# Performance work log

Hardware: AMD Instinct MI355X
Metric: run time of the kernel (lower is better)

## Reference

```python
import jax, jax.numpy as jnp
import numpy as np

N_NODES = 50000
IN_CH = 128
HID = 128
OUT_CH = 40
N_LAYERS = 3
N_EDGES = 600000


def setup_inputs() -> dict:
    key = jax.random.key(0)
    ks = jax.random.split(key, 4 + 5 * N_LAYERS)
    x = jax.random.normal(ks[0], (N_NODES, IN_CH), dtype=jnp.float32)
    edge_attr = jax.random.normal(ks[1], (N_EDGES, 4), dtype=jnp.float32)
    edge_index = jax.random.randint(ks[2], (2, N_EDGES), 0, N_NODES, dtype=jnp.int64)
    # Per-layer MLP params ([in->hid->hid]); in==hid so stack as [L, d, d].
    def glorot(k, fan_in, fan_out):
        s = jnp.sqrt(2.0 / (fan_in + fan_out)).astype(jnp.float32)
        return jax.random.normal(k, (fan_in, fan_out), dtype=jnp.float32) * s
    W1 = jnp.stack([glorot(ks[3 + i], IN_CH if i == 0 else HID, HID) for i in range(N_LAYERS)])
    b1 = jnp.zeros((N_LAYERS, HID), dtype=jnp.float32)
    W2 = jnp.stack([glorot(ks[3 + N_LAYERS + i], HID, HID) for i in range(N_LAYERS)])
    b2 = jnp.zeros((N_LAYERS, HID), dtype=jnp.float32)
    Wc = glorot(ks[3 + 2 * N_LAYERS], HID, OUT_CH)
    bc = jnp.zeros((OUT_CH,), dtype=jnp.float32)
    return {"x": x, "edge_attr": edge_attr, "edge_index": edge_index,
            "W1": W1, "b1": b1, "W2": W2, "b2": b2, "Wc": Wc, "bc": bc}


def reference(x, edge_attr, edge_index, W1, b1, W2, b2, Wc, bc):
    # GIN node classifier, eval mode (dropout = identity, BN = identity).
    src, dst = edge_index[0], edge_index[1]
    h = x
    for i in range(N_LAYERS):
        # GINConv (eps=0): aggregate sum of neighbor features via scatter-add.
        msgs = h[src]                                   # [E, d] gather
        aggr = jax.ops.segment_sum(msgs, dst, num_segments=N_NODES)  # [N, d]
        z = h + aggr                                    # (1+eps)*x + sum
        z = jax.nn.relu(z @ W1[i] + b1[i])              # MLP hidden
        z = z @ W2[i] + b2[i]                           # MLP out
        h = jax.nn.relu(z)                              # F.relu(conv(...))
    return h @ Wc + bc                                  # [N, OUT_CH]
```

## Files before the change

kernel.cpp:

```cpp
#include <hip/hip_runtime.h>

#define N_NODES 50000
#define IN_CH 128
#define HID 128
#define OUT_CH 40
#define N_LAYERS 3
#define N_EDGES 600000
#define DSTRIDE 64

typedef __attribute__((ext_vector_type(8))) short short8;
typedef __attribute__((ext_vector_type(4))) float floatx4;

static __device__ __forceinline__ unsigned short f32_to_bf16(float f) {
  unsigned u = __float_as_uint(f);
  unsigned r = 0x7FFFu + ((u >> 16) & 1u);
  return (unsigned short)((u + r) >> 16);
}
static __device__ __forceinline__ float bf16_to_f32(unsigned short h) {
  return __uint_as_float(((unsigned)h) << 16);
}

#define CONV_BLOCKS 6250
#define W_BLOCKS 408
#define DEG_BLOCKS 49
#define COL_MAX (N_NODES * DSTRIDE)
#define COLF_BLOCKS 3125

__global__ __launch_bounds__(256) void prep_all_kernel(
    const float* __restrict__ x, const float* __restrict__ W1,
    const float* __restrict__ W2, const float* __restrict__ Wc,
    unsigned short* __restrict__ xb, unsigned short* __restrict__ WT,
    unsigned short* __restrict__ WcT, unsigned short* __restrict__ hb1,
    int* __restrict__ deg, int* __restrict__ col) {
  const int b = blockIdx.x;
  const int t = threadIdx.x;
  if (b < CONV_BLOCKS) {
    int i = (b * 256 + t) * 4;
    if (i < N_NODES * 128) {
      float4 v = *(const float4*)(x + i);
      ushort4 o;
      o.x = f32_to_bf16(v.x); o.y = f32_to_bf16(v.y);
      o.z = f32_to_bf16(v.z); o.w = f32_to_bf16(v.w);
      *(ushort4*)(xb + i) = o;
    }
  } else if (b < CONV_BLOCKS + W_BLOCKS) {
    int o = (b - CONV_BLOCKS) * 256 + t;
    if (o < 6 * 16384) {
      int mat = o >> 14;
      int r = o & 16383;
      int n = r >> 7;
      int k = r & 127;
      const float* W = (mat < 3) ? (W1 + (size_t)mat * 16384)
                                 : (W2 + (size_t)(mat - 3) * 16384);
      WT[(size_t)mat * 16384 + (size_t)n * 128 + k] =
          f32_to_bf16(W[(size_t)k * 128 + n]);
    } else if (o < 6 * 16384 + 48 * 128) {
      int r = o - 6 * 16384;
      int n = r >> 7;
      int k = r & 127;
      float v = (n < OUT_CH) ? Wc[(size_t)k * OUT_CH + n] : 0.0f;
      WcT[(size_t)n * 128 + k] = f32_to_bf16(v);
    }
  } else if (b < CONV_BLOCKS + W_BLOCKS + DEG_BLOCKS) {
    int i = ((b - CONV_BLOCKS - W_BLOCKS) * 256 + t) * 4;
    if (i + 3 < N_NODES) {
      *(int4*)(deg + i) = make_int4(0, 0, 0, 0);
    } else {
      for (int k = 0; k < 4; ++k)
        if (i + k < N_NODES) deg[i + k] = 0;
    }
  } else if (b < CONV_BLOCKS + W_BLOCKS + DEG_BLOCKS + COLF_BLOCKS) {
    int i = ((b - CONV_BLOCKS - W_BLOCKS - DEG_BLOCKS) * 256 + t) * 4;
    *(int4*)(col + i) = make_int4(N_NODES, N_NODES, N_NODES, N_NODES);
  } else {
    if (t < 128) xb[(size_t)N_NODES * 128 + t] = 0;
    else hb1[(size_t)N_NODES * 128 + (t - 128)] = 0;
  }
}

__global__ __launch_bounds__(256) void csr_kernel(
    const int* __restrict__ ei, int* __restrict__ deg, int* __restrict__ col) {
  int e = blockIdx.x * 256 + threadIdx.x;
  if (e >= N_EDGES) return;
  int s = ei[e];
  int d = ei[N_EDGES + e];
  int pos = atomicAdd(&deg[d], 1);
  col[(size_t)d * DSTRIDE + pos] = s;
}

__global__ __launch_bounds__(256) void aggregate_kernel(
    const unsigned short* __restrict__ h, const int* __restrict__ deg,
    const int* __restrict__ col, unsigned short* __restrict__ z) {
  int n = __builtin_amdgcn_readfirstlane(blockIdx.x * 4 + (threadIdx.x >> 6));
  int q = threadIdx.x & 63;
  const size_t co = (size_t)q * 2;
  ushort2 sv = *(const ushort2*)(h + (size_t)n * 128 + co);
  float ax[8], ay[8];
#pragma unroll
  for (int k = 0; k < 8; ++k) { ax[k] = 0.f; ay[k] = 0.f; }
  ax[0] = bf16_to_f32(sv.x);
  ay[0] = bf16_to_f32(sv.y);
  int dg = __builtin_amdgcn_readfirstlane(deg[n]);
  int cnt = (dg + 15) & ~15;
  const int* cp = col + (size_t)n * DSTRIDE;
  for (int i = 0; i < cnt; i += 16) {
    int ss[16];
#pragma unroll
    for (int k = 0; k < 16; ++k)
      ss[k] = __builtin_amdgcn_readfirstlane(cp[i + k]);
    ushort2 vv[16];
#pragma unroll
    for (int k = 0; k < 16; ++k)
      vv[k] = *(const ushort2*)(h + (size_t)ss[k] * 128 + co);
#pragma unroll
    for (int k = 0; k < 16; ++k) {
      ax[k & 7] += bf16_to_f32(vv[k].x);
      ay[k & 7] += bf16_to_f32(vv[k].y);
    }
  }
  float s0 = (ax[0] + ax[1]) + (ax[2] + ax[3]) + (ax[4] + ax[5]) + (ax[6] + ax[7]);
  float s1 = (ay[0] + ay[1]) + (ay[2] + ay[3]) + (ay[4] + ay[5]) + (ay[6] + ay[7]);
  ushort2 o;
  o.x = f32_to_bf16(s0);
  o.y = f32_to_bf16(s1);
  *(ushort2*)(z + (size_t)n * 128 + co) = o;
}

template <bool LAST>
__global__ __launch_bounds__(256) void layer_pair_kernel(
    const unsigned short* __restrict__ A, const unsigned short* __restrict__ WT1,
    const float* __restrict__ b1, const unsigned short* __restrict__ WT2,
    const float* __restrict__ b2, unsigned short* __restrict__ Z,
    const unsigned short* __restrict__ WcT, const float* __restrict__ bc,
    float* __restrict__ out, int M) {
  __shared__ __align__(16) unsigned short Wl[128][136];
  __shared__ __align__(16) unsigned short T[64][136];
  const int tid = threadIdx.x;
  const int w = tid >> 6;
  const int lane = tid & 63;
  const int qg = lane >> 4;
  const int ln = lane & 15;
  const int row0 = blockIdx.x * 64;
  const int rbase = w * 16;
  const int r0 = row0 + rbase + ln;
  const short8 zero8 = {0, 0, 0, 0, 0, 0, 0, 0};

#pragma unroll
  for (int j = 0; j < 8; ++j) {
    int slot = tid + j * 256;
    int row = slot >> 4;
    int kb = slot & 15;
    *(short8*)&Wl[row][kb * 8] = *(const short8*)(WT1 + (size_t)row * 128 + kb * 8);
  }
  __syncthreads();

  floatx4 acc[8];
#pragma unroll
  for (int ct = 0; ct < 8; ++ct) acc[ct] = (floatx4){0.f, 0.f, 0.f, 0.f};
#pragma unroll
  for (int ks = 0; ks < 4; ++ks) {
    const int koff = ks * 32 + qg * 8;
    short8 a = (r0 < M) ? *(const short8*)(A + (size_t)r0 * 128 + koff) : zero8;
#pragma unroll
    for (int ct = 0; ct < 8; ++ct) {
      short8 b = *(const short8*)&Wl[ct * 16 + ln][koff];
      acc[ct] = __builtin_amdgcn_mfma_f32_16x16x32_bf16(a, b, acc[ct], 0, 0, 0);
    }
  }
#pragma unroll
  for (int ct = 0; ct < 8; ++ct) {
    float bv = b1[ct * 16 + ln];
#pragma unroll
    for (int r = 0; r < 4; ++r) {
      float v = fmaxf(acc[ct][r] + bv, 0.0f);
      T[rbase + qg * 4 + r][ct * 16 + ln] = f32_to_bf16(v);
    }
  }

  __syncthreads();
#pragma unroll
  for (int j = 0; j < 8; ++j) {
    int slot = tid + j * 256;
    int row = slot >> 4;
    int kb = slot & 15;
    *(short8*)&Wl[row][kb * 8] = *(const short8*)(WT2 + (size_t)row * 128 + kb * 8);
  }
  __syncthreads();

  floatx4 acc2[8];
#pragma unroll
  for (int ct = 0; ct < 8; ++ct) acc2[ct] = (floatx4){0.f, 0.f, 0.f, 0.f};
#pragma unroll
  for (int ks = 0; ks < 4; ++ks) {
    const int koff = ks * 32 + qg * 8;
    short8 a = *(const short8*)&T[rbase + ln][koff];
#pragma unroll
    for (int ct = 0; ct < 8; ++ct) {
      short8 b = *(const short8*)&Wl[ct * 16 + ln][koff];
      acc2[ct] = __builtin_amdgcn_mfma_f32_16x16x32_bf16(a, b, acc2[ct], 0, 0, 0);
    }
  }
#pragma unroll
  for (int ct = 0; ct < 8; ++ct) {
    float bv = b2[ct * 16 + ln];
#pragma unroll
    for (int r = 0; r < 4; ++r) {
      float v = fmaxf(acc2[ct][r] + bv, 0.0f);
      T[rbase + qg * 4 + r][ct * 16 + ln] = f32_to_bf16(v);
    }
  }

  if (LAST) {
    floatx4 acc3[3];
#pragma unroll
    for (int ct = 0; ct < 3; ++ct) acc3[ct] = (floatx4){0.f, 0.f, 0.f, 0.f};
#pragma unroll
    for (int ks = 0; ks < 4; ++ks) {
      const int koff = ks * 32 + qg * 8;
      short8 a = *(const short8*)&T[rbase + ln][koff];
#pragma unroll
      for (int ct = 0; ct < 3; ++ct) {
        short8 b = *(const short8*)(WcT + (size_t)(ct * 16 + ln) * 128 + koff);
        acc3[ct] = __builtin_amdgcn_mfma_f32_16x16x32_bf16(a, b, acc3[ct], 0, 0, 0);
      }
    }
#pragma unroll
    for (int ct = 0; ct < 3; ++ct) {
      int colg = ct * 16 + ln;
      if (colg < OUT_CH) {
        float bv = bc[colg];
#pragma unroll
        for (int r = 0; r < 4; ++r) {
          int row = row0 + rbase + qg * 4 + r;
          if (row < M) out[(size_t)row * OUT_CH + colg] = acc3[ct][r] + bv;
        }
      }
    }
  } else {
    __syncthreads();
#pragma unroll
    for (int j = 0; j < 4; ++j) {
      int slot = tid + j * 256;
      int row = slot >> 4;
      int kb = slot & 15;
      if (row0 + row < M) {
        short8 v = *(const short8*)&T[row][kb * 8];
        *(short8*)(Z + (size_t)(row0 + row) * 128 + kb * 8) = v;
      }
    }
  }
}

extern "C" void kernel_launch(void* const* d_in, const int* in_sizes, int n_in,
                              void* d_out, int out_size, void* d_ws,
                              size_t ws_size, hipStream_t stream) {
  const float* x = (const float*)d_in[0];
  const int* ei = (const int*)d_in[2];
  const float* W1 = (const float*)d_in[3];
  const float* b1 = (const float*)d_in[4];
  const float* W2 = (const float*)d_in[5];
  const float* b2 = (const float*)d_in[6];
  const float* Wc = (const float*)d_in[7];
  const float* bc = (const float*)d_in[8];
  float* out = (float*)d_out;

  const size_t NF = (size_t)(N_NODES + 1) * 128;
  unsigned short* hb0 = (unsigned short*)d_ws;
  unsigned short* hb1 = hb0 + NF;
  unsigned short* xbf = hb1 + NF;
  unsigned short* WT = xbf + NF;
  unsigned short* WcT = WT + 6 * 16384;
  int* deg = (int*)(WcT + 48 * 128);
  int* col = deg + N_NODES;

  const dim3 blk(256);
  const int edge_grid = (N_EDGES + 255) / 256;
  const int aggr_grid = N_NODES / 4;
  const int pair_grid = (N_NODES + 63) / 64;

  prep_all_kernel<<<CONV_BLOCKS + W_BLOCKS + DEG_BLOCKS + COLF_BLOCKS + 1, blk,
                    0, stream>>>(x, W1, W2, Wc, xbf, WT, WcT, hb1, deg, col);

  csr_kernel<<<edge_grid, blk, 0, stream>>>(ei, deg, col);

  const unsigned short* h = xbf;
  for (int l = 0; l < N_LAYERS; ++l) {
    aggregate_kernel<<<aggr_grid, blk, 0, stream>>>(h, deg, col, hb0);
    if (l < N_LAYERS - 1) {
      layer_pair_kernel<false><<<pair_grid, blk, 0, stream>>>(
          hb0, WT + (size_t)l * 16384, b1 + (size_t)l * 128,
          WT + (size_t)(3 + l) * 16384, b2 + (size_t)l * 128, hb1,
          nullptr, nullptr, nullptr, N_NODES);
      h = hb1;
    } else {
      layer_pair_kernel<true><<<pair_grid, blk, 0, stream>>>(
          hb0, WT + (size_t)l * 16384, b1 + (size_t)l * 128,
          WT + (size_t)(3 + l) * 16384, b2 + (size_t)l * 128, nullptr,
          WcT, bc, out, N_NODES);
    }
  }
}
```

Measured before the change: 245.2 us.

## Pad degree counters, drop col prefill, and batch four edges per CSR thread

Degree counters are now spaced 32 ints apart so atomics on different nodes land on separate 128-byte lines. The full fill of the col array with a sentinel is removed; the aggregate kernel instead masks slots beyond the node's degree to the zero row. The CSR build processes four edges per thread with vectorized int4 loads. In exchange, the deg array grows from 50K to 1.6M ints and must still be zeroed, which adds prep write traffic.

```diff
diff --git a/kernel.cpp b/kernel.cpp
--- a/kernel.cpp
+++ b/kernel.cpp
@@ -7,6 +7,7 @@
 #define N_LAYERS 3
 #define N_EDGES 600000
 #define DSTRIDE 64
+#define DEGSTRIDE 32
 
 typedef __attribute__((ext_vector_type(8))) short short8;
 typedef __attribute__((ext_vector_type(4))) float floatx4;
@@ -22,16 +23,14 @@
 
 #define CONV_BLOCKS 6250
 #define W_BLOCKS 408
-#define DEG_BLOCKS 49
-#define COL_MAX (N_NODES * DSTRIDE)
-#define COLF_BLOCKS 3125
+#define DEG_BLOCKS 1563
 
 __global__ __launch_bounds__(256) void prep_all_kernel(
     const float* __restrict__ x, const float* __restrict__ W1,
     const float* __restrict__ W2, const float* __restrict__ Wc,
     unsigned short* __restrict__ xb, unsigned short* __restrict__ WT,
     unsigned short* __restrict__ WcT, unsigned short* __restrict__ hb1,
-    int* __restrict__ deg, int* __restrict__ col) {
+    int* __restrict__ deg) {
   const int b = blockIdx.x;
   const int t = threadIdx.x;
   if (b < CONV_BLOCKS) {
@@ -63,29 +62,28 @@
     }
   } else if (b < CONV_BLOCKS + W_BLOCKS + DEG_BLOCKS) {
     int i = ((b - CONV_BLOCKS - W_BLOCKS) * 256 + t) * 4;
-    if (i + 3 < N_NODES) {
-      *(int4*)(deg + i) = make_int4(0, 0, 0, 0);
-    } else {
-      for (int k = 0; k < 4; ++k)
-        if (i + k < N_NODES) deg[i + k] = 0;
-    }
-  } else if (b < CONV_BLOCKS + W_BLOCKS + DEG_BLOCKS + COLF_BLOCKS) {
-    int i = ((b - CONV_BLOCKS - W_BLOCKS - DEG_BLOCKS) * 256 + t) * 4;
-    *(int4*)(col + i) = make_int4(N_NODES, N_NODES, N_NODES, N_NODES);
+    if (i < N_NODES * DEGSTRIDE) *(int4*)(deg + i) = make_int4(0, 0, 0, 0);
   } else {
     if (t < 128) xb[(size_t)N_NODES * 128 + t] = 0;
     else hb1[(size_t)N_NODES * 128 + (t - 128)] = 0;
   }
 }
 
+#define CSR_BLOCKS 586
 __global__ __launch_bounds__(256) void csr_kernel(
     const int* __restrict__ ei, int* __restrict__ deg, int* __restrict__ col) {
-  int e = blockIdx.x * 256 + threadIdx.x;
-  if (e >= N_EDGES) return;
-  int s = ei[e];
-  int d = ei[N_EDGES + e];
-  int pos = atomicAdd(&deg[d], 1);
-  col[(size_t)d * DSTRIDE + pos] = s;
+  int base = (blockIdx.x * 256 + threadIdx.x) * 4;
+  if (base >= N_EDGES) return;
+  int4 s4 = *(const int4*)(ei + base);
+  int4 d4 = *(const int4*)(ei + N_EDGES + base);
+  int p0 = atomicAdd(&deg[(size_t)d4.x * DEGSTRIDE], 1);
+  int p1 = atomicAdd(&deg[(size_t)d4.y * DEGSTRIDE], 1);
+  int p2 = atomicAdd(&deg[(size_t)d4.z * DEGSTRIDE], 1);
+  int p3 = atomicAdd(&deg[(size_t)d4.w * DEGSTRIDE], 1);
+  col[(size_t)d4.x * DSTRIDE + p0] = s4.x;
+  col[(size_t)d4.y * DSTRIDE + p1] = s4.y;
+  col[(size_t)d4.z * DSTRIDE + p2] = s4.z;
+  col[(size_t)d4.w * DSTRIDE + p3] = s4.w;
 }
 
 __global__ __launch_bounds__(256) void aggregate_kernel(
@@ -100,14 +98,16 @@
   for (int k = 0; k < 8; ++k) { ax[k] = 0.f; ay[k] = 0.f; }
   ax[0] = bf16_to_f32(sv.x);
   ay[0] = bf16_to_f32(sv.y);
-  int dg = __builtin_amdgcn_readfirstlane(deg[n]);
+  int dg = __builtin_amdgcn_readfirstlane(deg[(size_t)n * DEGSTRIDE]);
   int cnt = (dg + 15) & ~15;
   const int* cp = col + (size_t)n * DSTRIDE;
   for (int i = 0; i < cnt; i += 16) {
     int ss[16];
 #pragma unroll
-    for (int k = 0; k < 16; ++k)
-      ss[k] = __builtin_amdgcn_readfirstlane(cp[i + k]);
+    for (int k = 0; k < 16; ++k) {
+      int sl = cp[i + k];
+      ss[k] = __builtin_amdgcn_readfirstlane((i + k < dg) ? sl : N_NODES);
+    }
     ushort2 vv[16];
 #pragma unroll
     for (int k = 0; k < 16; ++k)
@@ -271,17 +271,16 @@
   unsigned short* WT = xbf + NF;
   unsigned short* WcT = WT + 6 * 16384;
   int* deg = (int*)(WcT + 48 * 128);
-  int* col = deg + N_NODES;
+  int* col = deg + (size_t)N_NODES * DEGSTRIDE;
 
   const dim3 blk(256);
-  const int edge_grid = (N_EDGES + 255) / 256;
   const int aggr_grid = N_NODES / 4;
   const int pair_grid = (N_NODES + 63) / 64;
 
-  prep_all_kernel<<<CONV_BLOCKS + W_BLOCKS + DEG_BLOCKS + COLF_BLOCKS + 1, blk,
-                    0, stream>>>(x, W1, W2, Wc, xbf, WT, WcT, hb1, deg, col);
-
-  csr_kernel<<<edge_grid, blk, 0, stream>>>(ei, deg, col);
+  prep_all_kernel<<<CONV_BLOCKS + W_BLOCKS + DEG_BLOCKS + 1, blk, 0, stream>>>(
+      x, W1, W2, Wc, xbf, WT, WcT, hb1, deg);
+
+  csr_kernel<<<CSR_BLOCKS, blk, 0, stream>>>(ei, deg, col);
 
   const unsigned short* h = xbf;
   for (int l = 0; l < N_LAYERS; ++l) {
```

After: 245.5 us. About the same (+0.1%).
